# Optimization experiments

Hardware: AMD Instinct MI355X
Metric: run time of the kernel (lower is better)

Reference implementation:

```python
import jax, jax.numpy as jnp
import numpy as np

B, N = 8192, 2048


def setup_inputs() -> dict:
    key = jax.random.key(0)
    k1, k2 = jax.random.split(key)
    predictions = jax.random.normal(k1, (B, N), dtype=jnp.float32)
    targets = jax.random.normal(k2, (B, N), dtype=jnp.float32)
    return {"predictions": predictions, "targets": targets}


def reference(predictions, targets):
    # Original: per-batch NxN squared-difference cost matrix + scipy Hungarian,
    # then MSE(pred, optimally-permuted targets), averaged over the batch.
    # For scalar entries with cost (p_i - t_j)^2 the optimal assignment is the
    # monotone matching (rearrangement inequality): sort both vectors and pair
    # in order. This computes the exact same loss, fully vectorized.
    p_sorted = jnp.sort(predictions, axis=-1)  # [B, N]
    t_sorted = jnp.sort(targets, axis=-1)      # [B, N]
    # mean over N per row, then mean over B == global mean
    return jnp.mean((p_sorted - t_sorted) ** 2)
```

## Files before the change

kernel.cpp:

```cpp
#include <hip/hip_runtime.h>
#include <math.h>

#define ROWS 8192
#define NCOL 2048
#define V 32
#define WPB 4
#define THREADS (WPB * 64)

__device__ __forceinline__ void ce(float& a, float& b) {
  const float lo = fminf(a, b);
  const float hi = fmaxf(a, b);
  a = lo; b = hi;
}

__device__ __forceinline__ float ce_dir(float a, float b, float cdir) {
  return __builtin_amdgcn_fmed3f(a, b, cdir);
}

__device__ __forceinline__ float bperm(int addr, float x) {
  return __builtin_bit_cast(
      float, __builtin_amdgcn_ds_bpermute(addr, __builtin_bit_cast(int, x)));
}

__device__ __forceinline__ void sort_one(float (&x)[V], int lane) {
#pragma unroll
  for (int k = 2; k <= V; k <<= 1) {
#pragma unroll
    for (int v = 0; v < V; ++v) {
      if ((v & (k >> 1)) == 0) ce(x[v], x[v ^ (k - 1)]);
    }
#pragma unroll
    for (int j = k >> 2; j >= 1; j >>= 1) {
#pragma unroll
      for (int v = 0; v < V; ++v) {
        if ((v & j) == 0) ce(x[v], x[v | j]);
      }
    }
  }

#pragma unroll 1
  for (int kb = 1; kb <= 32; kb <<= 1) {
    {
      const int addr = ((lane ^ (2 * kb - 1)) << 2);
      const float cdir = (lane & kb) ? INFINITY : -INFINITY;
#pragma unroll
      for (int q = 0; q < 4; ++q) {
        const int vA = 4 * q;
        float o[8];
#pragma unroll
        for (int u = 0; u < 4; ++u) {
          o[u]     = bperm(addr, x[(vA + u) ^ 31]);
          o[u + 4] = bperm(addr, x[vA + u]);
        }
#pragma unroll
        for (int u = 0; u < 4; ++u) {
          x[vA + u]        = ce_dir(x[vA + u],        o[u],     cdir);
          x[(vA + u) ^ 31] = ce_dir(x[(vA + u) ^ 31], o[u + 4], cdir);
        }
      }
    }
#pragma unroll 1
    for (int m = kb >> 1; m >= 1; m >>= 1) {
      const int addr = ((lane ^ m) << 2);
      const float cdir = (lane & m) ? INFINITY : -INFINITY;
#pragma unroll
      for (int c = 0; c < V; c += 8) {
        float o[8];
#pragma unroll
        for (int u = 0; u < 8; ++u) o[u] = bperm(addr, x[c + u]);
#pragma unroll
        for (int u = 0; u < 8; ++u) x[c + u] = ce_dir(x[c + u], o[u], cdir);
      }
    }
#pragma unroll
    for (int j = 16; j >= 1; j >>= 1) {
#pragma unroll
      for (int v = 0; v < V; ++v) {
        if ((v & j) == 0) ce(x[v], x[v | j]);
      }
    }
  }
}

__global__ __launch_bounds__(THREADS, 2) void sort_mse_kernel(
    const float* __restrict__ pred, const float* __restrict__ targ,
    float* __restrict__ out) {
  const int lane = threadIdx.x & 63;
  const int wave = threadIdx.x >> 6;
  const int row = blockIdx.x * WPB + wave;
  const size_t base = (size_t)row * NCOL + (size_t)lane * V;

  float rp[V], rt[V];
  const float4* p4 = (const float4*)(pred + base);
  const float4* t4 = (const float4*)(targ + base);
#pragma unroll
  for (int q = 0; q < V / 4; ++q) {
    const float4 a = p4[q];
    rp[4 * q + 0] = a.x; rp[4 * q + 1] = a.y;
    rp[4 * q + 2] = a.z; rp[4 * q + 3] = a.w;
    const float4 b = t4[q];
    rt[4 * q + 0] = b.x; rt[4 * q + 1] = b.y;
    rt[4 * q + 2] = b.z; rt[4 * q + 3] = b.w;
  }

  sort_one(rp, lane);
  sort_one(rt, lane);

  float acc = 0.f;
#pragma unroll
  for (int v = 0; v < V; ++v) {
    const float d = rp[v] - rt[v];
    acc = fmaf(d, d, acc);
  }
#pragma unroll
  for (int off = 32; off > 0; off >>= 1) acc += __shfl_down(acc, off, 64);
  if (lane == 0) {
    unsafeAtomicAdd(out, acc * (1.0f / ((float)ROWS * (float)NCOL)));
  }
}

extern "C" void kernel_launch(void* const* d_in, const int* in_sizes, int n_in,
                              void* d_out, int out_size, void* d_ws, size_t ws_size,
                              hipStream_t stream) {
  const float* pred = (const float*)d_in[0];
  const float* targ = (const float*)d_in[1];
  float* out = (float*)d_out;

  hipMemsetAsync(out, 0, sizeof(float), stream);
  sort_mse_kernel<<<ROWS / WPB, THREADS, 0, stream>>>(pred, targ, out);
}
```

Before: 241.6 us.

## Split pred and target sorts across separate waves, combining via shared memory

```diff
diff --git a/kernel.cpp b/kernel.cpp
--- a/kernel.cpp
+++ b/kernel.cpp
@@ -4,8 +4,7 @@
 #define ROWS 8192
 #define NCOL 2048
 #define V 32
-#define WPB 4
-#define THREADS (WPB * 64)
+#define THREADS 256
 
 __device__ __forceinline__ void ce(float& a, float& b) {
   const float lo = fminf(a, b);
@@ -82,35 +81,51 @@
   }
 }
 
-__global__ __launch_bounds__(THREADS, 2) void sort_mse_kernel(
+__global__ __launch_bounds__(THREADS, 8) void sort_mse_kernel(
     const float* __restrict__ pred, const float* __restrict__ targ,
     float* __restrict__ out) {
   const int lane = threadIdx.x & 63;
   const int wave = threadIdx.x >> 6;
-  const int row = blockIdx.x * WPB + wave;
+  const int pair = wave & 1;
+  const int role = wave >> 1;
+  const int row = blockIdx.x * 2 + pair;
   const size_t base = (size_t)row * NCOL + (size_t)lane * V;
 
-  float rp[V], rt[V];
-  const float4* p4 = (const float4*)(pred + base);
-  const float4* t4 = (const float4*)(targ + base);
+  __shared__ float tbuf[2][NCOL];
+
+  float x[V];
+  const float4* s4 =
+      (const float4*)((role ? targ : pred) + base);
 #pragma unroll
   for (int q = 0; q < V / 4; ++q) {
-    const float4 a = p4[q];
-    rp[4 * q + 0] = a.x; rp[4 * q + 1] = a.y;
-    rp[4 * q + 2] = a.z; rp[4 * q + 3] = a.w;
-    const float4 b = t4[q];
-    rt[4 * q + 0] = b.x; rt[4 * q + 1] = b.y;
-    rt[4 * q + 2] = b.z; rt[4 * q + 3] = b.w;
+    const float4 a = s4[q];
+    x[4 * q + 0] = a.x; x[4 * q + 1] = a.y;
+    x[4 * q + 2] = a.z; x[4 * q + 3] = a.w;
   }
 
-  sort_one(rp, lane);
-  sort_one(rt, lane);
+  sort_one(x, lane);
+
+  if (role == 1) {
+#pragma unroll
+    for (int q = 0; q < V / 4; ++q) {
+      const int w = lane * V + 4 * (q ^ (lane & 7));
+      *(float4*)&tbuf[pair][w] =
+          make_float4(x[4 * q + 0], x[4 * q + 1], x[4 * q + 2], x[4 * q + 3]);
+    }
+  }
+  __syncthreads();
+  if (role == 1) return;
 
   float acc = 0.f;
 #pragma unroll
-  for (int v = 0; v < V; ++v) {
-    const float d = rp[v] - rt[v];
-    acc = fmaf(d, d, acc);
+  for (int q = 0; q < V / 4; ++q) {
+    const int w = lane * V + 4 * (q ^ (lane & 7));
+    const float4 t4 = *(const float4*)&tbuf[pair][w];
+    float d;
+    d = x[4 * q + 0] - t4.x; acc = fmaf(d, d, acc);
+    d = x[4 * q + 1] - t4.y; acc = fmaf(d, d, acc);
+    d = x[4 * q + 2] - t4.z; acc = fmaf(d, d, acc);
+    d = x[4 * q + 3] - t4.w; acc = fmaf(d, d, acc);
   }
 #pragma unroll
   for (int off = 32; off > 0; off >>= 1) acc += __shfl_down(acc, off, 64);
@@ -127,5 +142,5 @@
   float* out = (float*)d_out;
 
   hipMemsetAsync(out, 0, sizeof(float), stream);
-  sort_mse_kernel<<<ROWS / WPB, THREADS, 0, stream>>>(pred, targ, out);
+  sort_mse_kernel<<<ROWS / 2, THREADS, 0, stream>>>(pred, targ, out);
 }
```

Measured after the change: 233.9 us. 1.03x faster.
